# Kernel optimization log

Hardware: AMD Instinct MI355X
Metric: run time of the kernel (lower is better)

## Reference

```python
import jax, jax.numpy as jnp
import numpy as np

B, F, P, H, D = 2, 128, 256, 8, 64
DIM = H * D  # dim = num_heads * head_dim


def setup_inputs() -> dict:
    key = jax.random.key(0)
    ks = jax.random.split(key, 4)
    s = 0.02  # init scale for weights
    return {
        "x": jax.random.normal(ks[0], (B, F, P, DIM), jnp.float32),
        # frame QKV: projects dim -> (qkv, heads, dim_head)
        "W_f": (jax.random.normal(ks[1], (3, H, D, DIM), jnp.float32) * s),
        "b_f": jnp.zeros((3, H, D), jnp.float32),
        # point QKV: mixes (heads_in, dim_head_in) -> (qkv, heads_out, dim_head_out)
        "W_p": (jax.random.normal(ks[2], (3, H, D, H, D), jnp.float32) * s),
        "b_p": jnp.zeros((3, H, D), jnp.float32),
        # out projection: (heads, dim_head) -> dim
        "W_o": (jax.random.normal(ks[3], (H, D, DIM), jnp.float32) * s),
        "b_o": jnp.zeros((DIM,), jnp.float32),
    }


def reference(x, W_f, b_f, W_p, b_p, W_o, b_o):
    # ---- frame attention (attend across frames, per point) ----
    # qkv: [3, b, point, frame, heads, dim_head]
    qkv = jnp.einsum('bfpd,qhed->qbpfhe', x, W_f) + b_f[:, None, None, None, :, :]
    q, k, v = qkv[0], qkv[1], qkv[2]
    # scores: [b, point, frame_q, frame_k, heads]  (NOTE: source applies no 1/sqrt(d) scaling)
    scores = jnp.einsum('bpfhe,bpghe->bpfgh', q, k)
    w = jax.nn.softmax(scores, axis=3)  # softmax over frame_key
    fa = jnp.einsum('bpfgh,bpghe->bfphe', w, v)  # [b, frame, point, heads, dim_head]

    # ---- point attention (attend across points, per frame) ----
    # qkv2: [3, b, frame, point, heads, dim_head]
    qkv2 = jnp.einsum('bfpij,qheij->qbfphe', fa, W_p) + b_p[:, None, None, None, :, :]
    q2, k2, v2 = qkv2[0], qkv2[1], qkv2[2]
    # scores2: [b, frame, point_q, point_k, heads] (no scaling, per source)
    scores2 = jnp.einsum('bfphe,bfqhe->bfpqh', q2, k2)
    w2 = jax.nn.softmax(scores2, axis=3)  # softmax over point_key
    pa = jnp.einsum('bfpqh,bfqhe->bfphe', w2, v2)  # [b, frame, point, heads, dim_head]

    # ---- output projection ----
    return jnp.einsum('bfphe,hed->bfpd', pa, W_o) + b_o
```

## Files before the change

kernel.cpp:

```cpp
#include <hip/hip_runtime.h>
#include <hip/hip_bf16.h>
#include <stdint.h>

typedef __bf16 bf16;
typedef __attribute__((ext_vector_type(8))) __bf16 bf16x8;
typedef __attribute__((ext_vector_type(4))) __bf16 bf16x4;
typedef __attribute__((ext_vector_type(4))) float f32x4;

#define B_ 2
#define F_ 128
#define P_ 256
#define H_ 8
#define D_ 64
#define DIM_ 512
#define NROWS (B_*F_*P_)

__device__ __forceinline__ void load_lds16(const void* g, void* l) {
  __builtin_amdgcn_global_load_lds(
      (__attribute__((address_space(1))) void*)(uintptr_t)g,
      (__attribute__((address_space(3))) void*)(uint32_t)(uintptr_t)l,
      16, 0, 0);
}

__global__ void cvt_f32_bf16(const float* __restrict__ src, bf16* __restrict__ dst, int n)
{
  int i = (blockIdx.x * 256 + threadIdx.x) * 8;
  if (i < n) {
    float4 a = *(const float4*)(src + i);
    float4 b = *(const float4*)(src + i + 4);
    bf16x8 o;
    o[0] = (bf16)a.x; o[1] = (bf16)a.y; o[2] = (bf16)a.z; o[3] = (bf16)a.w;
    o[4] = (bf16)b.x; o[5] = (bf16)b.y; o[6] = (bf16)b.z; o[7] = (bf16)b.w;
    *(bf16x8*)(dst + i) = o;
  }
}

__global__ void transpose_wo(const float* __restrict__ src, bf16* __restrict__ dst)
{
  int idx = blockIdx.x * 256 + threadIdx.x;
  int d = idx & 511, he = idx >> 9;
  dst[(size_t)d * 512 + he] = (bf16)src[(size_t)he * 512 + d];
}

#define BM 128
#define BN 128
#define BK 32

template <typename OutT>
__global__ __launch_bounds__(256, 2)
void gemm_bt_bias(const bf16* __restrict__ A, const bf16* __restrict__ Bt,
                  const float* __restrict__ bias, OutT* __restrict__ C,
                  int N, int K)
{
  __shared__ __align__(16) bf16 As[BM * BK];
  __shared__ __align__(16) bf16 Bs[BN * BK];

  const int t    = threadIdx.x;
  const int lane = t & 63;
  const int wave = t >> 6;
  const int wm   = wave & 1;
  const int wn   = wave >> 1;
  const int l16  = lane & 15;
  const int qd   = lane >> 4;

  const int mBase = blockIdx.y * BM;
  const int nBase = blockIdx.x * BN;

  f32x4 acc[4][4] = {};

  for (int k0 = 0; k0 < K; k0 += BK) {
    __syncthreads();
#pragma unroll
    for (int r = 0; r < 2; ++r) {
      int c = r * 256 + t;
      int row = c >> 2;
      int col = (((c & 3) ^ (row & 3)) << 3);
      load_lds16(A  + (size_t)(mBase + row) * K + k0 + col, As + c * 8);
      load_lds16(Bt + (size_t)(nBase + row) * K + k0 + col, Bs + c * 8);
    }
    __syncthreads();

    bf16x8 a[4], b[4];
#pragma unroll
    for (int i = 0; i < 4; ++i) {
      int row = wm * 64 + i * 16 + l16;
      a[i] = *(const bf16x8*)(As + row * BK + ((qd ^ (row & 3)) << 3));
    }
#pragma unroll
    for (int j = 0; j < 4; ++j) {
      int row = wn * 64 + j * 16 + l16;
      b[j] = *(const bf16x8*)(Bs + row * BK + ((qd ^ (row & 3)) << 3));
    }
#pragma unroll
    for (int i = 0; i < 4; ++i)
#pragma unroll
      for (int j = 0; j < 4; ++j)
        acc[i][j] = __builtin_amdgcn_mfma_f32_16x16x32_bf16(a[i], b[j], acc[i][j], 0, 0, 0);
  }

#pragma unroll
  for (int j = 0; j < 4; ++j) {
    int coln = nBase + wn * 64 + j * 16 + l16;
    float bv = bias[coln];
#pragma unroll
    for (int i = 0; i < 4; ++i) {
      int rowm = mBase + wm * 64 + i * 16 + qd * 4;
#pragma unroll
      for (int r = 0; r < 4; ++r)
        C[(size_t)(rowm + r) * N + coln] = (OutT)(acc[i][j][r] + bv);
    }
  }
}

template <int NKT, int MODE, int VS>
__global__ __launch_bounds__(256, 2)
void attn2(const bf16* __restrict__ qkv, bf16* __restrict__ outp)
{
  __shared__ __align__(16) bf16 Vt[64 * VS];
  __shared__ __align__(16) bf16 Pq[128 * 136];

  const int t    = threadIdx.x;
  const int lane = t & 63;
  const int wave = t >> 6;
  const int l16  = lane & 15;
  const int qd   = lane >> 4;

  const int bid = blockIdx.x;
  int h, q0, rowbase, rstride;
  if (MODE == 0) {
    h = bid & 7;
    int p = (bid >> 3) & (P_ - 1);
    int b = bid >> 11;
    rowbase = b * F_ * P_ + p; rstride = P_; q0 = 0;
  } else {
    int qb = bid & 1;
    h = (bid >> 1) & 7;
    int f = (bid >> 4) & (F_ - 1);
    int b = bid >> 11;
    rowbase = (b * F_ + f) * P_; rstride = 1; q0 = qb * 128;
  }

#pragma unroll
  for (int p = 0; p < NKT / 8; ++p) {
    int key = p * 128 + (t >> 1);
    int eh  = (t & 1) * 32;
    const bf16* src = qkv + (size_t)(rowbase + key * rstride) * 1536 + 1024 + h * 64 + eh;
    bf16x8 v[4];
#pragma unroll
    for (int jj = 0; jj < 4; ++jj) v[jj] = *(const bf16x8*)(src + jj * 8);
#pragma unroll
    for (int jj = 0; jj < 4; ++jj)
#pragma unroll
      for (int j = 0; j < 8; ++j)
        Vt[(eh + jj * 8 + j) * VS + key] = v[jj][j];
  }

  const int qloc = wave * 32;
  bf16x8 qf[2][2];
#pragma unroll
  for (int qt = 0; qt < 2; ++qt)
#pragma unroll
    for (int ks = 0; ks < 2; ++ks)
      qf[qt][ks] = *(const bf16x8*)(qkv +
          (size_t)(rowbase + (q0 + qloc + qt * 16 + l16) * rstride) * 1536 +
          h * 64 + ks * 32 + qd * 8);

  f32x4 sacc[NKT][2] = {};
#pragma unroll
  for (int tn = 0; tn < NKT; ++tn) {
    const bf16* krow = qkv + (size_t)(rowbase + (tn * 16 + l16) * rstride) * 1536 + 512 + h * 64;
    bf16x8 kf0 = *(const bf16x8*)(krow + qd * 8);
    bf16x8 kf1 = *(const bf16x8*)(krow + 32 + qd * 8);
#pragma unroll
    for (int qt = 0; qt < 2; ++qt) {
      sacc[tn][qt] = __builtin_amdgcn_mfma_f32_16x16x32_bf16(kf0, qf[qt][0], sacc[tn][qt], 0, 0, 0);
      sacc[tn][qt] = __builtin_amdgcn_mfma_f32_16x16x32_bf16(kf1, qf[qt][1], sacc[tn][qt], 0, 0, 0);
    }
  }

#pragma unroll
  for (int qt = 0; qt < 2; ++qt) {
    float m = -3.0e38f;
#pragma unroll
    for (int tn = 0; tn < NKT; ++tn)
#pragma unroll
      for (int r = 0; r < 4; ++r) m = fmaxf(m, sacc[tn][qt][r]);
    m = fmaxf(m, __shfl_xor(m, 16));
    m = fmaxf(m, __shfl_xor(m, 32));
    float s = 0.0f;
#pragma unroll
    for (int tn = 0; tn < NKT; ++tn)
#pragma unroll
      for (int r = 0; r < 4; ++r) {
        float e0 = __expf(sacc[tn][qt][r] - m);
        sacc[tn][qt][r] = e0;
        s += e0;
      }
    s += __shfl_xor(s, 16);
    s += __shfl_xor(s, 32);
    float inv = 1.0f / s;
#pragma unroll
    for (int tn = 0; tn < NKT; ++tn)
#pragma unroll
      for (int r = 0; r < 4; ++r) sacc[tn][qt][r] *= inv;
  }

  f32x4 oacc[4][2] = {};
#pragma unroll
  for (int hf = 0; hf < NKT / 8; ++hf) {
#pragma unroll
    for (int qt = 0; qt < 2; ++qt)
#pragma unroll
      for (int tl = 0; tl < 8; ++tl) {
        int tn = hf * 8 + tl;
        bf16x4 pk;
#pragma unroll
        for (int r = 0; r < 4; ++r) pk[r] = (bf16)sacc[tn][qt][r];
        *(bf16x4*)(Pq + (qloc + qt * 16 + l16) * 136 + tl * 16 + qd * 4) = pk;
      }
    if (hf == 0) __syncthreads();
#pragma unroll
    for (int ks = 0; ks < 4; ++ks) {
      bf16x8 pf[2];
#pragma unroll
      for (int qt = 0; qt < 2; ++qt)
        pf[qt] = *(const bf16x8*)(Pq + (qloc + qt * 16 + l16) * 136 + ks * 32 + qd * 8);
#pragma unroll
      for (int te = 0; te < 4; ++te) {
        bf16x8 vf = *(const bf16x8*)(Vt + (te * 16 + l16) * VS + hf * 128 + ks * 32 + qd * 8);
#pragma unroll
        for (int qt = 0; qt < 2; ++qt)
          oacc[te][qt] = __builtin_amdgcn_mfma_f32_16x16x32_bf16(vf, pf[qt], oacc[te][qt], 0, 0, 0);
      }
    }
  }

#pragma unroll
  for (int te = 0; te < 4; ++te)
#pragma unroll
    for (int qt = 0; qt < 2; ++qt) {
      int q = q0 + qloc + qt * 16 + l16;
      bf16x4 pk;
#pragma unroll
      for (int r = 0; r < 4; ++r) pk[r] = (bf16)oacc[te][qt][r];
      *(bf16x4*)(outp + (size_t)(rowbase + q * rstride) * 512 + h * 64 + te * 16 + qd * 4) = pk;
    }
}

extern "C" void kernel_launch(void* const* d_in, const int* in_sizes, int n_in,
                              void* d_out, int out_size, void* d_ws, size_t ws_size,
                              hipStream_t stream)
{
  (void)in_sizes; (void)n_in; (void)out_size; (void)ws_size;
  const float* x   = (const float*)d_in[0];
  const float* Wf  = (const float*)d_in[1];
  const float* bfb = (const float*)d_in[2];
  const float* Wp  = (const float*)d_in[3];
  const float* bpb = (const float*)d_in[4];
  const float* Wo  = (const float*)d_in[5];
  const float* bob = (const float*)d_in[6];
  float* out = (float*)d_out;

  char* ws = (char*)d_ws;
  bf16* qkv = (bf16*)ws;
  bf16* fa  = (bf16*)(ws + (size_t)NROWS * 1536 * 2);
  bf16* xb  = fa;
  char* wbase = ws + (size_t)NROWS * 1536 * 2 + (size_t)NROWS * 512 * 2;
  bf16* wfb = (bf16*)wbase;
  bf16* wpb = (bf16*)(wbase + 1536 * 512 * 2);
  bf16* wot = (bf16*)(wbase + 2 * 1536 * 512 * 2);

  cvt_f32_bf16<<<(NROWS * 512) / (256 * 8), 256, 0, stream>>>(x, xb, NROWS * 512);
  cvt_f32_bf16<<<(1536 * 512) / (256 * 8), 256, 0, stream>>>(Wf, wfb, 1536 * 512);
  cvt_f32_bf16<<<(1536 * 512) / (256 * 8), 256, 0, stream>>>(Wp, wpb, 1536 * 512);
  transpose_wo<<<1024, 256, 0, stream>>>(Wo, wot);

  gemm_bt_bias<bf16><<<dim3(12, 512), 256, 0, stream>>>(xb, wfb, bfb, qkv, 1536, 512);
  attn2<8, 0, 136><<<4096, 256, 0, stream>>>(qkv, fa);
  gemm_bt_bias<bf16><<<dim3(12, 512), 256, 0, stream>>>(fa, wpb, bpb, qkv, 1536, 512);
  attn2<16, 1, 272><<<4096, 256, 0, stream>>>(qkv, fa);
  gemm_bt_bias<float><<<dim3(4, 512), 256, 0, stream>>>(fa, wot, bob, out, 512, 512);
}
```

Measured before the change: 771.1 us.

## Replace GEMM with 256x256 tile kernel using 4-stage async LDS pipeline

Replaces the 128x128 tile, 256-thread GEMM with a 512-thread, 256x256 tile kernel. It streams K-tiles through a 4-deep LDS ring buffer using global_load_lds, with explicit vmcnt waits and split A/B staging around the MFMA phases. It also remaps block IDs in an XCD-aware order and raises wave priority during MFMA bursts. The goal is more data reuse per byte loaded and hiding global-load latency behind compute. The cost is 128KB of LDS per block, which limits occupancy to one block per CU, and hardcoded K=512 and vmcnt counts that are fragile.

```diff
diff --git a/kernel.cpp b/kernel.cpp
--- a/kernel.cpp
+++ b/kernel.cpp
@@ -42,69 +42,106 @@
   dst[(size_t)d * 512 + he] = (bf16)src[(size_t)he * 512 + d];
 }
 
-#define BM 128
-#define BN 128
-#define BK 32
-
-template <typename OutT>
-__global__ __launch_bounds__(256, 2)
-void gemm_bt_bias(const bf16* __restrict__ A, const bf16* __restrict__ Bt,
-                  const float* __restrict__ bias, OutT* __restrict__ C,
-                  int N, int K)
-{
-  __shared__ __align__(16) bf16 As[BM * BK];
-  __shared__ __align__(16) bf16 Bs[BN * BK];
+template <typename OutT, int NT>
+__global__ __launch_bounds__(512, 2)
+void gemm256(const bf16* __restrict__ A, const bf16* __restrict__ Bt,
+             const float* __restrict__ bias, OutT* __restrict__ C)
+{
+  constexpr int K = 512;
+  constexpr int N = NT * 256;
+  constexpr int NTILES = 16;
+  __shared__ __align__(16) bf16 As[4][256 * 32];
+  __shared__ __align__(16) bf16 Bs[4][256 * 32];
 
   const int t    = threadIdx.x;
   const int lane = t & 63;
-  const int wave = t >> 6;
-  const int wm   = wave & 1;
-  const int wn   = wave >> 1;
   const int l16  = lane & 15;
   const int qd   = lane >> 4;
-
-  const int mBase = blockIdx.y * BM;
-  const int nBase = blockIdx.x * BN;
-
-  f32x4 acc[4][4] = {};
-
-  for (int k0 = 0; k0 < K; k0 += BK) {
-    __syncthreads();
-#pragma unroll
-    for (int r = 0; r < 2; ++r) {
-      int c = r * 256 + t;
-      int row = c >> 2;
-      int col = (((c & 3) ^ (row & 3)) << 3);
-      load_lds16(A  + (size_t)(mBase + row) * K + k0 + col, As + c * 8);
-      load_lds16(Bt + (size_t)(nBase + row) * K + k0 + col, Bs + c * 8);
-    }
-    __syncthreads();
+  const int wave = t >> 6;
+  const int wm   = wave >> 2;
+  const int wn   = wave & 3;
+
+  constexpr int NWG = NT * 256;
+  const int logical = (blockIdx.x & 7) * (NWG / 8) + (blockIdx.x >> 3);
+  const int mBase = (logical / NT) * 256;
+  const int nBase = (logical % NT) * 256;
+
+  const int srow = t >> 2;
+  const int soct = (((t & 3) ^ ((srow >> 1) & 3)) << 3);
+  const bf16* aS0 = A  + (size_t)(mBase + srow)       * K + soct;
+  const bf16* aS1 = A  + (size_t)(mBase + srow + 128) * K + soct;
+  const bf16* bS0 = Bt + (size_t)(nBase + srow)       * K + soct;
+  const bf16* bS1 = Bt + (size_t)(nBase + srow + 128) * K + soct;
+  const int dst = t * 8;
+
+#define STAGE_A(tt) do { \
+    load_lds16(aS0 + (tt) * 32, &As[(tt) & 3][dst]); \
+    load_lds16(aS1 + (tt) * 32, &As[(tt) & 3][4096 + dst]); } while (0)
+#define STAGE_B(tt) do { \
+    load_lds16(bS0 + (tt) * 32, &Bs[(tt) & 3][dst]); \
+    load_lds16(bS1 + (tt) * 32, &Bs[(tt) & 3][4096 + dst]); } while (0)
+
+  const int swz = ((qd ^ ((l16 >> 1) & 3)) << 3);
+  const bf16* aRd = &As[0][(wm * 128 + l16) * 32 + swz];
+  const bf16* bRd = &Bs[0][(wn * 64  + l16) * 32 + swz];
+
+  f32x4 acc[8][4] = {};
+
+  STAGE_A(0); STAGE_B(0); STAGE_A(1); STAGE_B(1); STAGE_A(2); STAGE_B(2);
+
+#define MF(i, j, av, bv) \
+  acc[i][j] = __builtin_amdgcn_mfma_f32_16x16x32_bf16(av, bv, acc[i][j], 0, 0, 0)
+
+#pragma unroll
+  for (int tt = 0; tt < NTILES; ++tt) {
+    if (tt + 3 < NTILES) STAGE_A(tt + 3);
+    if      (tt <= NTILES - 4) asm volatile("s_waitcnt vmcnt(10)" ::: "memory");
+    else if (tt == NTILES - 3) asm volatile("s_waitcnt vmcnt(8)"  ::: "memory");
+    else if (tt == NTILES - 2) asm volatile("s_waitcnt vmcnt(4)"  ::: "memory");
+    else                       asm volatile("s_waitcnt vmcnt(0)"  ::: "memory");
+    __builtin_amdgcn_s_barrier();
+    asm volatile("" ::: "memory");
+
+    const bf16* aB = aRd + (tt & 3) * (256 * 32);
+    const bf16* bB = bRd + (tt & 3) * (256 * 32);
 
     bf16x8 a[4], b[4];
 #pragma unroll
-    for (int i = 0; i < 4; ++i) {
-      int row = wm * 64 + i * 16 + l16;
-      a[i] = *(const bf16x8*)(As + row * BK + ((qd ^ (row & 3)) << 3));
-    }
-#pragma unroll
-    for (int j = 0; j < 4; ++j) {
-      int row = wn * 64 + j * 16 + l16;
-      b[j] = *(const bf16x8*)(Bs + row * BK + ((qd ^ (row & 3)) << 3));
-    }
+    for (int j = 0; j < 4; ++j) b[j] = *(const bf16x8*)(bB + j * 512);
+#pragma unroll
+    for (int i = 0; i < 4; ++i) a[i] = *(const bf16x8*)(aB + i * 512);
+    __builtin_amdgcn_s_setprio(1);
 #pragma unroll
     for (int i = 0; i < 4; ++i)
 #pragma unroll
-      for (int j = 0; j < 4; ++j)
-        acc[i][j] = __builtin_amdgcn_mfma_f32_16x16x32_bf16(a[i], b[j], acc[i][j], 0, 0, 0);
-  }
+      for (int j = 0; j < 4; ++j) MF(i, j, a[i], b[j]);
+    __builtin_amdgcn_s_setprio(0);
+    __builtin_amdgcn_s_barrier();
+    asm volatile("" ::: "memory");
+
+    if (tt + 3 < NTILES) STAGE_B(tt + 3);
+#pragma unroll
+    for (int i = 0; i < 4; ++i) a[i] = *(const bf16x8*)(aB + (4 + i) * 512);
+    __builtin_amdgcn_s_setprio(1);
+#pragma unroll
+    for (int i = 0; i < 4; ++i)
+#pragma unroll
+      for (int j = 0; j < 4; ++j) MF(4 + i, j, a[i], b[j]);
+    __builtin_amdgcn_s_setprio(0);
+    __builtin_amdgcn_s_barrier();
+    asm volatile("" ::: "memory");
+  }
+#undef STAGE_A
+#undef STAGE_B
+#undef MF
 
 #pragma unroll
   for (int j = 0; j < 4; ++j) {
-    int coln = nBase + wn * 64 + j * 16 + l16;
-    float bv = bias[coln];
-#pragma unroll
-    for (int i = 0; i < 4; ++i) {
-      int rowm = mBase + wm * 64 + i * 16 + qd * 4;
+    const int coln = nBase + wn * 64 + j * 16 + l16;
+    const float bv = bias[coln];
+#pragma unroll
+    for (int i = 0; i < 8; ++i) {
+      const int rowm = mBase + wm * 128 + i * 16 + qd * 4;
 #pragma unroll
       for (int r = 0; r < 4; ++r)
         C[(size_t)(rowm + r) * N + coln] = (OutT)(acc[i][j][r] + bv);
@@ -275,9 +312,9 @@
   cvt_f32_bf16<<<(1536 * 512) / (256 * 8), 256, 0, stream>>>(Wp, wpb, 1536 * 512);
   transpose_wo<<<1024, 256, 0, stream>>>(Wo, wot);
 
-  gemm_bt_bias<bf16><<<dim3(12, 512), 256, 0, stream>>>(xb, wfb, bfb, qkv, 1536, 512);
+  gemm256<bf16, 6><<<1536, 512, 0, stream>>>(xb, wfb, bfb, qkv);
   attn2<8, 0, 136><<<4096, 256, 0, stream>>>(qkv, fa);
-  gemm_bt_bias<bf16><<<dim3(12, 512), 256, 0, stream>>>(fa, wpb, bpb, qkv, 1536, 512);
+  gemm256<bf16, 6><<<1536, 512, 0, stream>>>(fa, wpb, bpb, qkv);
   attn2<16, 1, 272><<<4096, 256, 0, stream>>>(qkv, fa);
-  gemm_bt_bias<float><<<dim3(4, 512), 256, 0, stream>>>(fa, wot, bob, out, 512, 512);
-}
+  gemm256<float, 2><<<512, 512, 0, stream>>>(fa, wot, bob, out);
+}
```

New measurement: 744.7 us. 3.4% less time.

## Replace GEMM with triple-buffered 256x128 pipelined kernel and vectorized epilogue

Applied to the files above, without the earlier changes.

Replaces the simple double-sync GEMM with a 512-thread kernel that computes 256x128 tiles and fixes K at 512. LDS is triple-buffered and filled two tiles ahead with async global-to-LDS loads, using explicit vmcnt waits and raw barriers instead of __syncthreads. Block indices are remapped across XCDs for better L2 locality, and wave priority is raised around the MFMA block. The MFMA operands are swapped so each lane holds contiguous output columns, which allows vectorized bias loads and 4-wide stores. The cost is roughly 73KB of LDS per block, which limits occupancy, and fragile hand-written wait counts.

```diff
diff --git a/kernel.cpp b/kernel.cpp
--- a/kernel.cpp
+++ b/kernel.cpp
@@ -42,72 +42,99 @@
   dst[(size_t)d * 512 + he] = (bf16)src[(size_t)he * 512 + d];
 }
 
-#define BM 128
-#define BN 128
-#define BK 32
-
-template <typename OutT>
-__global__ __launch_bounds__(256, 2)
-void gemm_bt_bias(const bf16* __restrict__ A, const bf16* __restrict__ Bt,
-                  const float* __restrict__ bias, OutT* __restrict__ C,
-                  int N, int K)
-{
-  __shared__ __align__(16) bf16 As[BM * BK];
-  __shared__ __align__(16) bf16 Bs[BN * BK];
+template <typename OutT, int NTn>
+__global__ __launch_bounds__(512, 4)
+void gemm_mn(const bf16* __restrict__ A, const bf16* __restrict__ Bt,
+             const float* __restrict__ bias, OutT* __restrict__ C)
+{
+  constexpr int K = 512;
+  constexpr int N = NTn * 128;
+  constexpr int NTILES = 16;
+  constexpr int BUF = 12288;
+  __shared__ __align__(16) bf16 Ls[3 * BUF];
 
   const int t    = threadIdx.x;
   const int lane = t & 63;
-  const int wave = t >> 6;
-  const int wm   = wave & 1;
-  const int wn   = wave >> 1;
   const int l16  = lane & 15;
   const int qd   = lane >> 4;
-
-  const int mBase = blockIdx.y * BM;
-  const int nBase = blockIdx.x * BN;
+  const int wave = t >> 6;
+  const int wm   = wave >> 1;
+  const int wn   = wave & 1;
+
+  constexpr int NWG = 256 * NTn;
+  const int logical = (blockIdx.x & 7) * (NWG / 8) + (blockIdx.x >> 3);
+  const int mBase = (logical / NTn) * 256;
+  const int nBase = (logical % NTn) * 128;
+
+  const int soct = (((t & 3) ^ ((t >> 3) & 3)) << 3);
+  const bf16* aP0 = A  + (size_t)(mBase + (t >> 2)) * K + soct;
+  const bf16* aP1 = aP0 + (size_t)128 * K;
+  const bf16* bP  = Bt + (size_t)(nBase + (t >> 2)) * K + soct;
+
+#define STAGE(tt) do { bf16* Lb_ = Ls + ((tt) % 3) * BUF; \
+    load_lds16(aP0 + (tt) * 32, Lb_ + t * 8); \
+    load_lds16(aP1 + (tt) * 32, Lb_ + 4096 + t * 8); \
+    load_lds16(bP  + (tt) * 32, Lb_ + 8192 + t * 8); } while (0)
+
+  const int swz    = ((qd ^ ((l16 >> 1) & 3)) << 3);
+  const int aRdOff = (wm * 64 + l16) * 32 + swz;
+  const int bRdOff = 8192 + (wn * 64 + l16) * 32 + swz;
 
   f32x4 acc[4][4] = {};
 
-  for (int k0 = 0; k0 < K; k0 += BK) {
-    __syncthreads();
-#pragma unroll
-    for (int r = 0; r < 2; ++r) {
-      int c = r * 256 + t;
-      int row = c >> 2;
-      int col = (((c & 3) ^ (row & 3)) << 3);
-      load_lds16(A  + (size_t)(mBase + row) * K + k0 + col, As + c * 8);
-      load_lds16(Bt + (size_t)(nBase + row) * K + k0 + col, Bs + c * 8);
-    }
-    __syncthreads();
-
+#define MF(i, j, av, bv) \
+  acc[i][j] = __builtin_amdgcn_mfma_f32_16x16x32_bf16(av, bv, acc[i][j], 0, 0, 0)
+
+  STAGE(0); STAGE(1);
+
+#pragma unroll
+  for (int tt = 0; tt < NTILES; ++tt) {
+    if (tt + 2 < NTILES) STAGE(tt + 2);
+    if      (tt <  NTILES - 2) asm volatile("s_waitcnt vmcnt(6)" ::: "memory");
+    else if (tt == NTILES - 2) asm volatile("s_waitcnt vmcnt(3)" ::: "memory");
+    else                       asm volatile("s_waitcnt vmcnt(0)" ::: "memory");
+    __builtin_amdgcn_s_barrier();
+    asm volatile("" ::: "memory");
+
+    const bf16* Lb = Ls + (tt % 3) * BUF;
     bf16x8 a[4], b[4];
 #pragma unroll
+    for (int j = 0; j < 4; ++j) b[j] = *(const bf16x8*)(Lb + bRdOff + j * 512);
+#pragma unroll
+    for (int i = 0; i < 4; ++i) a[i] = *(const bf16x8*)(Lb + aRdOff + i * 512);
+
+    __builtin_amdgcn_s_setprio(1);
+#pragma unroll
+    for (int i = 0; i < 4; ++i)
+#pragma unroll
+      for (int j = 0; j < 4; ++j) MF(i, j, b[j], a[i]);
+    __builtin_amdgcn_s_setprio(0);
+
+    asm volatile("s_waitcnt lgkmcnt(0)" ::: "memory");
+    __builtin_amdgcn_s_barrier();
+    asm volatile("" ::: "memory");
+  }
+#undef STAGE
+#undef MF
+
+#pragma unroll
+  for (int j = 0; j < 4; ++j) {
+    const int ncol = nBase + wn * 64 + j * 16 + qd * 4;
+    const f32x4 bv = *(const f32x4*)(bias + ncol);
+#pragma unroll
     for (int i = 0; i < 4; ++i) {
-      int row = wm * 64 + i * 16 + l16;
-      a[i] = *(const bf16x8*)(As + row * BK + ((qd ^ (row & 3)) << 3));
-    }
-#pragma unroll
-    for (int j = 0; j < 4; ++j) {
-      int row = wn * 64 + j * 16 + l16;
-      b[j] = *(const bf16x8*)(Bs + row * BK + ((qd ^ (row & 3)) << 3));
-    }
-#pragma unroll
-    for (int i = 0; i < 4; ++i)
-#pragma unroll
-      for (int j = 0; j < 4; ++j)
-        acc[i][j] = __builtin_amdgcn_mfma_f32_16x16x32_bf16(a[i], b[j], acc[i][j], 0, 0, 0);
-  }
-
-#pragma unroll
-  for (int j = 0; j < 4; ++j) {
-    int coln = nBase + wn * 64 + j * 16 + l16;
-    float bv = bias[coln];
-#pragma unroll
-    for (int i = 0; i < 4; ++i) {
-      int rowm = mBase + wm * 64 + i * 16 + qd * 4;
-#pragma unroll
-      for (int r = 0; r < 4; ++r)
-        C[(size_t)(rowm + r) * N + coln] = (OutT)(acc[i][j][r] + bv);
+      const size_t off = (size_t)(mBase + wm * 64 + i * 16 + l16) * N + ncol;
+      if constexpr (__is_same(OutT, float)) {
+        f32x4 o;
+#pragma unroll
+        for (int r = 0; r < 4; ++r) o[r] = acc[i][j][r] + bv[r];
+        *(f32x4*)(C + off) = o;
+      } else {
+        bf16x4 o;
+#pragma unroll
+        for (int r = 0; r < 4; ++r) o[r] = (bf16)(acc[i][j][r] + bv[r]);
+        *(bf16x4*)(C + off) = o;
+      }
     }
   }
 }
@@ -275,9 +302,9 @@
   cvt_f32_bf16<<<(1536 * 512) / (256 * 8), 256, 0, stream>>>(Wp, wpb, 1536 * 512);
   transpose_wo<<<1024, 256, 0, stream>>>(Wo, wot);
 
-  gemm_bt_bias<bf16><<<dim3(12, 512), 256, 0, stream>>>(xb, wfb, bfb, qkv, 1536, 512);
+  gemm_mn<bf16, 12><<<3072, 512, 0, stream>>>(xb, wfb, bfb, qkv);
   attn2<8, 0, 136><<<4096, 256, 0, stream>>>(qkv, fa);
-  gemm_bt_bias<bf16><<<dim3(12, 512), 256, 0, stream>>>(fa, wpb, bpb, qkv, 1536, 512);
+  gemm_mn<bf16, 12><<<3072, 512, 0, stream>>>(fa, wpb, bpb, qkv);
   attn2<16, 1, 272><<<4096, 256, 0, stream>>>(qkv, fa);
-  gemm_bt_bias<float><<<dim3(4, 512), 256, 0, stream>>>(fa, wot, bob, out, 512, 512);
-}
+  gemm_mn<float, 4><<<1024, 512, 0, stream>>>(fa, wot, bob, out);
+}
```

New measurement: 783.5 us. About the same (+1.6%).
